# Performance work log

Hardware: AMD Instinct MI355X
Metric: run time of the kernel (lower is better)

Reference implementation:

```python
import jax, jax.numpy as jnp
import numpy as np

D_MODEL = 512
N_HEADS = 8
B, S = 4, 1024
REL_HIDDEN = 64


def setup_inputs() -> dict:
    key = jax.random.key(0)
    ks = jax.random.split(key, 16)

    def g(k, shape, scale=0.02):
        return jax.random.normal(k, shape, dtype=jnp.float32) * scale

    x = jax.random.normal(ks[0], (B, S, D_MODEL), dtype=jnp.float32)
    freqs = jax.random.uniform(ks[1], (B, S, 1), dtype=jnp.float32)
    return {
        "x": x,
        "freqs": freqs,
        "Wq": g(ks[2], (D_MODEL, D_MODEL)), "bq": g(ks[3], (D_MODEL,)),
        "Wk": g(ks[4], (D_MODEL, D_MODEL)), "bk": g(ks[5], (D_MODEL,)),
        "Wv": g(ks[6], (D_MODEL, D_MODEL)), "bv": g(ks[7], (D_MODEL,)),
        "Wo": g(ks[8], (D_MODEL, D_MODEL)), "bo": g(ks[9], (D_MODEL,)),
        "W1": g(ks[10], (2, REL_HIDDEN)), "b1": g(ks[11], (REL_HIDDEN,)),
        "W2": g(ks[12], (REL_HIDDEN, N_HEADS)), "b2": g(ks[13], (N_HEADS,)),
    }


def reference(x, freqs, Wq, bq, Wk, bk, Wv, bv, Wo, bo, W1, b1, W2, b2):
    b, s, d = x.shape
    h = N_HEADS
    dh = d // h

    def proj(W, bias):  # (b,s,d) -> (b,h,s,dh)
        return (x @ W + bias).reshape(b, s, h, dh).transpose(0, 2, 1, 3)

    Q = proj(Wq, bq)
    K = proj(Wk, bk)
    V = proj(Wv, bv)

    scores = jnp.einsum('bhid,bhjd->bhij', Q, K) / jnp.sqrt(jnp.float32(dh))

    # per-pair relative-frequency features: (b,s,s,2)
    eps = 1e-6
    fd = freqs[:, :, None, :] - freqs[:, None, :, :]
    fr = jnp.log((freqs[:, :, None, :] + eps) / (freqs[:, None, :, :] + eps))
    rel = jnp.concatenate([fd, fr], axis=-1)

    # MLP bias -> (b,s,s,h) -> (b,h,s,s)
    bias = jax.nn.relu(rel @ W1 + b1) @ W2 + b2
    scores = scores + jnp.transpose(bias, (0, 3, 1, 2))

    attn = jax.nn.softmax(scores, axis=-1)
    ctx = jnp.einsum('bhij,bhjd->bhid', attn, V)
    ctx = ctx.transpose(0, 2, 1, 3).reshape(b, s, d)
    return ctx @ Wo + bo
```

## Files before the change

kernel.cpp:

```cpp
#include <hip/hip_runtime.h>
#include <hip/hip_bf16.h>
#include <cstdint>

#define BATCH   4
#define SEQ     1024
#define DM      512
#define NH      8
#define DH      64
#define RH      64

typedef float f32x4 __attribute__((ext_vector_type(4)));
typedef __bf16 bf16x8 __attribute__((ext_vector_type(8)));

#define QB_OFF    (0)
#define KB_OFF    (4  << 20)
#define VT_OFF    (8  << 20)
#define XB_OFF    (12 << 20)
#define WT_OFF    (16 << 20)
#define WOT_OFF   (18 << 20)
#define W2T_OFF   (19 << 20)
#define AW_OFF    (20 << 20)
#define CW_OFF    (21 << 20)
#define CTXB_OFF  (22 << 20)
#define BIAS_OFF  (32 << 20)

__global__ __launch_bounds__(256) void cast_x(
    const float* __restrict__ x, __bf16* __restrict__ xb)
{
    const size_t i = ((size_t)blockIdx.x * 256 + threadIdx.x) * 8;
    const float4 a = *(const float4*)&x[i];
    const float4 b = *(const float4*)&x[i + 4];
    bf16x8 o;
    o[0] = (__bf16)a.x; o[1] = (__bf16)a.y; o[2] = (__bf16)a.z; o[3] = (__bf16)a.w;
    o[4] = (__bf16)b.x; o[5] = (__bf16)b.y; o[6] = (__bf16)b.z; o[7] = (__bf16)b.w;
    *(bf16x8*)&xb[i] = o;
}

__global__ __launch_bounds__(256) void cast_w(
    const float* __restrict__ Wq, const float* __restrict__ Wk,
    const float* __restrict__ Wv, const float* __restrict__ Wo,
    __bf16* __restrict__ Wt, __bf16* __restrict__ Wot)
{
    const int t = threadIdx.x;
    const int k0 = blockIdx.x * 64;
    const int n0 = blockIdx.y * 64;
    const int z  = blockIdx.z;
    const float* __restrict__ src = (z == 0) ? Wq : (z == 1) ? Wk : (z == 2) ? Wv : Wo;
    __bf16* __restrict__ dst = (z < 3) ? (Wt + (size_t)(z * 512 + n0) * 512)
                                       : (Wot + (size_t)n0 * 512);

    __shared__ __align__(16) float Ts[64][65];
    #pragma unroll
    for (int i = 0; i < 4; ++i) {
        const int id = t + i * 256;
        const int row = id >> 4, c4 = (id & 15) * 4;
        const float4 v = *(const float4*)&src[(size_t)(k0 + row) * DM + n0 + c4];
        Ts[row][c4 + 0] = v.x; Ts[row][c4 + 1] = v.y;
        Ts[row][c4 + 2] = v.z; Ts[row][c4 + 3] = v.w;
    }
    __syncthreads();
    #pragma unroll
    for (int i = 0; i < 2; ++i) {
        const int id = t + i * 256;
        const int rn = id >> 3, ck = (id & 7) * 8;
        bf16x8 o;
        #pragma unroll
        for (int j = 0; j < 8; ++j) o[j] = (__bf16)Ts[ck + j][rn];
        *(bf16x8*)&dst[(size_t)rn * 512 + k0 + ck] = o;
    }
}

__global__ __launch_bounds__(256) void w2t_kernel(
    const float* __restrict__ W2, __bf16* __restrict__ W2t)
{
    const int t = threadIdx.x;
    #pragma unroll
    for (int r = 0; r < 4; ++r) {
        const int id = t + r * 256;
        const int h = id >> 6, k = id & 63;
        W2t[id] = (h < NH) ? (__bf16)W2[k * NH + h] : (__bf16)0.f;
    }
}

__global__ __launch_bounds__(256) void gemm_qkv_mfma(
    const __bf16* __restrict__ xb, const __bf16* __restrict__ Wt,
    const float* __restrict__ bq, const float* __restrict__ bk,
    const float* __restrict__ bv,
    __bf16* __restrict__ Qb, __bf16* __restrict__ Kb, __bf16* __restrict__ Vtb)
{
    const int t = threadIdx.x;
    const int wave = t >> 6, lane = t & 63;
    const int wm = wave >> 1, wn = wave & 1;
    const int r = lane & 15, kc = lane >> 4, q4 = kc * 4;
    const int m0 = blockIdx.y * 128;
    const int n0 = blockIdx.x * 128;
    const int sec = n0 >> 9;
    const int nn = n0 & 511;

    __shared__ __align__(16) char smem[36864];
    __bf16* __restrict__ As = (__bf16*)smem;
    __bf16* __restrict__ Bs = (__bf16*)(smem + 18432);

    f32x4 acc[4][4];
    #pragma unroll
    for (int i = 0; i < 4; ++i)
        #pragma unroll
        for (int j = 0; j < 4; ++j) acc[i][j] = {0.f, 0.f, 0.f, 0.f};

    const int srow = t >> 3, sck = (t & 7) * 8;
    const __bf16* __restrict__ Ag = xb + (size_t)(m0 + srow) * 512 + sck;
    const __bf16* __restrict__ Bg = Wt + (size_t)(n0 + srow) * 512 + sck;

    for (int k0 = 0; k0 < 512; k0 += 64) {
        bf16x8 ra[4], rb[4];
        #pragma unroll
        for (int i = 0; i < 4; ++i) {
            ra[i] = *(const bf16x8*)(Ag + (size_t)i * 32 * 512 + k0);
            rb[i] = *(const bf16x8*)(Bg + (size_t)i * 32 * 512 + k0);
        }
        __syncthreads();
        #pragma unroll
        for (int i = 0; i < 4; ++i) {
            *(bf16x8*)&As[(srow + i * 32) * 72 + sck] = ra[i];
            *(bf16x8*)&Bs[(srow + i * 32) * 72 + sck] = rb[i];
        }
        __syncthreads();
        #pragma unroll
        for (int ks = 0; ks < 2; ++ks) {
            bf16x8 af[4], bf[4];
            #pragma unroll
            for (int mf = 0; mf < 4; ++mf)
                af[mf] = *(const bf16x8*)&As[(wm * 64 + mf * 16 + r) * 72 + ks * 32 + kc * 8];
            #pragma unroll
            for (int nf = 0; nf < 4; ++nf)
                bf[nf] = *(const bf16x8*)&Bs[(wn * 64 + nf * 16 + r) * 72 + ks * 32 + kc * 8];
            #pragma unroll
            for (int mf = 0; mf < 4; ++mf)
                #pragma unroll
                for (int nf = 0; nf < 4; ++nf)
                    acc[mf][nf] = __builtin_amdgcn_mfma_f32_16x16x32_bf16(
                        af[mf], bf[nf], acc[mf][nf], 0, 0, 0);
        }
    }

    const float* __restrict__ bias = (sec == 0) ? bq : (sec == 1) ? bk : bv;
    __syncthreads();
    __bf16* __restrict__ Ls = (__bf16*)smem;
    if (sec < 2) {
        #pragma unroll
        for (int mf = 0; mf < 4; ++mf)
            #pragma unroll
            for (int nf = 0; nf < 4; ++nf) {
                const int n_l = wn * 64 + nf * 16 + r;
                const float bb = bias[nn + n_l];
                #pragma unroll
                for (int rr = 0; rr < 4; ++rr)
                    Ls[(wm * 64 + mf * 16 + q4 + rr) * 136 + n_l] =
                        (__bf16)(acc[mf][nf][rr] + bb);
            }
    } else {
        #pragma unroll
        for (int mf = 0; mf < 4; ++mf)
            #pragma unroll
            for (int nf = 0; nf < 4; ++nf) {
                const int n_l = wn * 64 + nf * 16 + r;
                const float bb = bias[nn + n_l];
                #pragma unroll
                for (int rr = 0; rr < 4; ++rr)
                    Ls[n_l * 136 + (wm * 64 + mf * 16 + q4 + rr)] =
                        (__bf16)(acc[mf][nf][rr] + bb);
            }
    }
    __syncthreads();

    const int b = m0 >> 10, sbase = m0 & 1023;
    if (sec < 2) {
        __bf16* __restrict__ dst = sec ? Kb : Qb;
        #pragma unroll
        for (int i = 0; i < 8; ++i) {
            const int id = t + i * 256;
            const int row = id >> 4, nc = (id & 15) * 8;
            const bf16x8 v = *(const bf16x8*)&Ls[row * 136 + nc];
            const int ng = nn + nc, h = ng >> 6, c = ng & 63;
            *(bf16x8*)&dst[((size_t)(b * NH + h) * SEQ + sbase + row) * DH + c] = v;
        }
    } else {
        #pragma unroll
        for (int i = 0; i < 8; ++i) {
            const int id = t + i * 256;
            const int nrow = id >> 4, mc = (id & 15) * 8;
            const bf16x8 v = *(const bf16x8*)&Ls[nrow * 136 + mc];
            const int ng = nn + nrow, h = ng >> 6, c = ng & 63;
            *(bf16x8*)&Vtb[((size_t)(b * NH + h) * DH + c) * SEQ + sbase + mc] = v;
        }
    }
}

__global__ __launch_bounds__(256) void gemm_out_mfma(
    const __bf16* __restrict__ ctxb, const __bf16* __restrict__ Wot,
    const float* __restrict__ bo, float* __restrict__ out)
{
    const int t = threadIdx.x;
    const int wave = t >> 6, lane = t & 63;
    const int wm = wave >> 1, wn = wave & 1;
    const int r = lane & 15, kc = lane >> 4, q4 = kc * 4;
    const int m0 = blockIdx.y * 128;
    const int n0 = blockIdx.x * 128;

    __shared__ __align__(16) char smem[36864];
    __bf16* __restrict__ As = (__bf16*)smem;
    __bf16* __restrict__ Bs = (__bf16*)(smem + 18432);

    f32x4 acc[4][4];
    #pragma unroll
    for (int i = 0; i < 4; ++i)
        #pragma unroll
        for (int j = 0; j < 4; ++j) acc[i][j] = {0.f, 0.f, 0.f, 0.f};

    const int srow = t >> 3, sck = (t & 7) * 8;
    const __bf16* __restrict__ Ag = ctxb + (size_t)(m0 + srow) * 512 + sck;
    const __bf16* __restrict__ Bg = Wot + (size_t)(n0 + srow) * 512 + sck;

    for (int k0 = 0; k0 < 512; k0 += 64) {
        bf16x8 ra[4], rb[4];
        #pragma unroll
        for (int i = 0; i < 4; ++i) {
            ra[i] = *(const bf16x8*)(Ag + (size_t)i * 32 * 512 + k0);
            rb[i] = *(const bf16x8*)(Bg + (size_t)i * 32 * 512 + k0);
        }
        __syncthreads();
        #pragma unroll
        for (int i = 0; i < 4; ++i) {
            *(bf16x8*)&As[(srow + i * 32) * 72 + sck] = ra[i];
            *(bf16x8*)&Bs[(srow + i * 32) * 72 + sck] = rb[i];
        }
        __syncthreads();
        #pragma unroll
        for (int ks = 0; ks < 2; ++ks) {
            bf16x8 af[4], bf[4];
            #pragma unroll
            for (int mf = 0; mf < 4; ++mf)
                af[mf] = *(const bf16x8*)&As[(wm * 64 + mf * 16 + r) * 72 + ks * 32 + kc * 8];
            #pragma unroll
            for (int nf = 0; nf < 4; ++nf)
                bf[nf] = *(const bf16x8*)&Bs[(wn * 64 + nf * 16 + r) * 72 + ks * 32 + kc * 8];
            #pragma unroll
            for (int mf = 0; mf < 4; ++mf)
                #pragma unroll
                for (int nf = 0; nf < 4; ++nf)
                    acc[mf][nf] = __builtin_amdgcn_mfma_f32_16x16x32_bf16(
                        af[mf], bf[nf], acc[mf][nf], 0, 0, 0);
        }
    }

    #pragma unroll
    for (int mf = 0; mf < 4; ++mf)
        #pragma unroll
        for (int nf = 0; nf < 4; ++nf) {
            const int n_l = wn * 64 + nf * 16 + r;
            const float bb = bo[n0 + n_l];
            #pragma unroll
            for (int rr = 0; rr < 4; ++rr)
                out[(size_t)(m0 + wm * 64 + mf * 16 + q4 + rr) * DM + n0 + n_l] =
                    acc[mf][nf][rr] + bb;
        }
}

__global__ __launch_bounds__(64) void rel_kernel(
    const float* __restrict__ freqs,
    const float* __restrict__ W1,
    const float* __restrict__ b1,
    float* __restrict__ Aw,
    float* __restrict__ Cw)
{
    const int row = blockIdx.x;
    const int k = threadIdx.x;
    const float f = freqs[row];
    const float L = logf(f + 1e-6f);
    const float base = f * W1[k] + L * W1[RH + k];
    Aw[(size_t)row * RH + k] = base + b1[k];
    Cw[(size_t)row * RH + k] = -base;
}

__global__ __launch_bounds__(256) void bias_mfma(
    const float* __restrict__ Aw, const float* __restrict__ Cw,
    const __bf16* __restrict__ W2t, __bf16* __restrict__ biasb)
{
    const int t = threadIdx.x;
    const int wave = t >> 6, lane = t & 63;
    const int jl = lane & 15, kc = lane >> 4;
    const int j0 = blockIdx.x * 128;
    const int i0 = blockIdx.y * 16;
    const int b  = blockIdx.z;

    __shared__ __align__(16) float Cs[128][68];

    {
        const int jr = t >> 1, half = (t & 1) * 32;
        const float* __restrict__ src = &Cw[((size_t)b * SEQ + j0 + jr) * RH + half];
        #pragma unroll
        for (int q = 0; q < 8; ++q) {
            const float4 v = *(const float4*)(src + q * 4);
            *(float4*)&Cs[jr][half + q * 4] = v;
        }
    }

    const bf16x8 w2f0 = *(const bf16x8*)&W2t[jl * 64 + kc * 8];
    const bf16x8 w2f1 = *(const bf16x8*)&W2t[jl * 64 + 32 + kc * 8];

    __syncthreads();

    const int iw = i0 + wave * 4;
    #pragma unroll
    for (int ii = 0; ii < 4; ++ii) {
        const int i = iw + ii;
        const float* __restrict__ ap = &Aw[((size_t)b * SEQ + i) * RH];
        const float4 a0 = *(const float4*)(ap + kc * 8);
        const float4 a1 = *(const float4*)(ap + kc * 8 + 4);
        const float4 a2 = *(const float4*)(ap + 32 + kc * 8);
        const float4 a3 = *(const float4*)(ap + 32 + kc * 8 + 4);

        #pragma unroll
        for (int jt = 0; jt < 8; ++jt) {
            const float* __restrict__ cp = &Cs[jt * 16 + jl][kc * 8];
            f32x4 acc = {0.f, 0.f, 0.f, 0.f};

            const float4 c0 = *(const float4*)(cp);
            const float4 c1 = *(const float4*)(cp + 4);
            bf16x8 hb0;
            hb0[0] = (__bf16)fmaxf(a0.x + c0.x, 0.f);
            hb0[1] = (__bf16)fmaxf(a0.y + c0.y, 0.f);
            hb0[2] = (__bf16)fmaxf(a0.z + c0.z, 0.f);
            hb0[3] = (__bf16)fmaxf(a0.w + c0.w, 0.f);
            hb0[4] = (__bf16)fmaxf(a1.x + c1.x, 0.f);
            hb0[5] = (__bf16)fmaxf(a1.y + c1.y, 0.f);
            hb0[6] = (__bf16)fmaxf(a1.z + c1.z, 0.f);
            hb0[7] = (__bf16)fmaxf(a1.w + c1.w, 0.f);
            acc = __builtin_amdgcn_mfma_f32_16x16x32_bf16(w2f0, hb0, acc, 0, 0, 0);

            const float4 c2 = *(const float4*)(cp + 32);
            const float4 c3 = *(const float4*)(cp + 36);
            bf16x8 hb1;
            hb1[0] = (__bf16)fmaxf(a2.x + c2.x, 0.f);
            hb1[1] = (__bf16)fmaxf(a2.y + c2.y, 0.f);
            hb1[2] = (__bf16)fmaxf(a2.z + c2.z, 0.f);
            hb1[3] = (__bf16)fmaxf(a2.w + c2.w, 0.f);
            hb1[4] = (__bf16)fmaxf(a3.x + c3.x, 0.f);
            hb1[5] = (__bf16)fmaxf(a3.y + c3.y, 0.f);
            hb1[6] = (__bf16)fmaxf(a3.z + c3.z, 0.f);
            hb1[7] = (__bf16)fmaxf(a3.w + c3.w, 0.f);
            acc = __builtin_amdgcn_mfma_f32_16x16x32_bf16(w2f1, hb1, acc, 0, 0, 0);

            if (kc < 2) {
                #pragma unroll
                for (int rr = 0; rr < 4; ++rr)
                    biasb[(((size_t)b * NH + kc * 4 + rr) * SEQ + i) * SEQ
                          + j0 + jt * 16 + jl] = (__bf16)acc[rr];
            }
        }
    }
}

#define SSTR 1028
#define PSTR 1032

__global__ __launch_bounds__(512) void attn_mfma(
    const __bf16* __restrict__ Qb, const __bf16* __restrict__ Kb,
    const __bf16* __restrict__ Vtb, const __bf16* __restrict__ biasb,
    __bf16* __restrict__ ctxb)
{
    const int t = threadIdx.x;
    const int wave = t >> 6, lane = t & 63;
    const int r = lane & 15, kc = lane >> 4;
    const int blk = blockIdx.x;
    const int it = blk & 63;
    const int h  = (blk >> 6) & 7;
    const int b  = blk >> 9;
    const int s0 = it * 16;
    const int bh = b * NH + h;

    __shared__ __align__(16) float Ss[16 * SSTR];
    __shared__ float invl[16];

    const int prow = t >> 5, pln = t & 31;
    const __bf16* __restrict__ bpre =
        biasb + ((size_t)bh * SEQ + s0 + prow) * SEQ + pln * 8;
    const bf16x8 bre0 = *(const bf16x8*)(bpre);
    const bf16x8 bre1 = *(const bf16x8*)(bpre + 256);
    const bf16x8 bre2 = *(const bf16x8*)(bpre + 512);
    const bf16x8 bre3 = *(const bf16x8*)(bpre + 768);

    {
        const __bf16* __restrict__ Qp = Qb + ((size_t)bh * SEQ + s0) * DH;
        const __bf16* __restrict__ Kp = Kb + (size_t)bh * SEQ * DH;
        const bf16x8 qa0 = *(const bf16x8*)(Qp + r * DH + kc * 8);
        const bf16x8 qa1 = *(const bf16x8*)(Qp + r * DH + 32 + kc * 8);
        __builtin_amdgcn_s_setprio(1);
        #pragma unroll
        for (int jt = 0; jt < 8; ++jt) {
            const int j0 = wave * 128 + jt * 16;
            const bf16x8 kb0 = *(const bf16x8*)(Kp + (size_t)(j0 + r) * DH + kc * 8);
            const bf16x8 kb1 = *(const bf16x8*)(Kp + (size_t)(j0 + r) * DH + 32 + kc * 8);
            f32x4 acc = {0.f, 0.f, 0.f, 0.f};
            acc = __builtin_amdgcn_mfma_f32_16x16x32_bf16(qa0, kb0, acc, 0, 0, 0);
            acc = __builtin_amdgcn_mfma_f32_16x16x32_bf16(qa1, kb1, acc, 0, 0, 0);
            #pragma unroll
            for (int rr = 0; rr < 4; ++rr)
                Ss[(kc * 4 + rr) * SSTR + j0 + r] = acc[rr] * 0.125f;
        }
        __builtin_amdgcn_s_setprio(0);
    }
    __syncthreads();

    {
        const float* __restrict__ sp = &Ss[prow * SSTR + pln * 8];
        float sv[32];
        float m = -1e30f;
        #pragma unroll
        for (int c = 0; c < 4; ++c) {
            const float4 sa = *(const float4*)(sp + c * 256);
            const float4 sb = *(const float4*)(sp + c * 256 + 4);
            const bf16x8 br = (c == 0) ? bre0 : (c == 1) ? bre1 : (c == 2) ? bre2 : bre3;
            float s;
            s = sa.x + (float)br[0]; sv[c * 8 + 0] = s; m = fmaxf(m, s);
            s = sa.y + (float)br[1]; sv[c * 8 + 1] = s; m = fmaxf(m, s);
            s = sa.z + (float)br[2]; sv[c * 8 + 2] = s; m = fmaxf(m, s);
            s = sa.w + (float)br[3]; sv[c * 8 + 3] = s; m = fmaxf(m, s);
            s = sb.x + (float)br[4]; sv[c * 8 + 4] = s; m = fmaxf(m, s);
            s = sb.y + (float)br[5]; sv[c * 8 + 5] = s; m = fmaxf(m, s);
            s = sb.z + (float)br[6]; sv[c * 8 + 6] = s; m = fmaxf(m, s);
            s = sb.w + (float)br[7]; sv[c * 8 + 7] = s; m = fmaxf(m, s);
        }
        #pragma unroll
        for (int mask = 16; mask >= 1; mask >>= 1)
            m = fmaxf(m, __shfl_xor(m, mask));
        float l = 0.f;
        #pragma unroll
        for (int jj = 0; jj < 32; ++jj) {
            const float p = __expf(sv[jj] - m);
            sv[jj] = p;
            l += p;
        }
        #pragma unroll
        for (int mask = 16; mask >= 1; mask >>= 1)
            l += __shfl_xor(l, mask);
        if (pln == 0) invl[prow] = 1.0f / l;
        __syncthreads();
        __bf16* __restrict__ Pb = (__bf16*)Ss;
        #pragma unroll
        for (int c = 0; c < 4; ++c) {
            bf16x8 pv;
            #pragma unroll
            for (int e = 0; e < 8; ++e) pv[e] = (__bf16)sv[c * 8 + e];
            *(bf16x8*)&Pb[prow * PSTR + c * 256 + pln * 8] = pv;
        }
    }
    __syncthreads();

    {
        const int ct = wave & 3, kh = wave >> 2;
        const __bf16* __restrict__ Pb = (const __bf16*)Ss;
        const __bf16* __restrict__ Vp =
            Vtb + ((size_t)bh * DH + ct * 16 + r) * SEQ + kh * 512;
        f32x4 acc = {0.f, 0.f, 0.f, 0.f};
        __builtin_amdgcn_s_setprio(1);
        #pragma unroll 4
        for (int jt = 0; jt < 16; ++jt) {
            const bf16x8 pa = *(const bf16x8*)(Pb + (size_t)r * PSTR + kh * 512 + jt * 32 + kc * 8);
            const bf16x8 vb = *(const bf16x8*)(Vp + jt * 32 + kc * 8);
            acc = __builtin_amdgcn_mfma_f32_16x16x32_bf16(pa, vb, acc, 0, 0, 0);
        }
        __builtin_amdgcn_s_setprio(0);
        float* __restrict__ part = Ss + 8256;
        if (kh == 1) {
            #pragma unroll
            for (int rr = 0; rr < 4; ++rr)
                part[ct * 272 + (kc * 4 + rr) * 17 + r] = acc[rr];
        }
        __syncthreads();
        if (kh == 0) {
            #pragma unroll
            for (int rr = 0; rr < 4; ++rr) {
                const int row = kc * 4 + rr;
                const float v = (acc[rr] + part[ct * 272 + row * 17 + r]) * invl[row];
                ctxb[((size_t)(b * SEQ) + s0 + row) * DM + h * DH + ct * 16 + r] = (__bf16)v;
            }
        }
    }
}

extern "C" void kernel_launch(void* const* d_in, const int* in_sizes, int n_in,
                              void* d_out, int out_size, void* d_ws, size_t ws_size,
                              hipStream_t stream)
{
    const float* x     = (const float*)d_in[0];
    const float* freqs = (const float*)d_in[1];
    const float* Wq    = (const float*)d_in[2];
    const float* bq    = (const float*)d_in[3];
    const float* Wk    = (const float*)d_in[4];
    const float* bk    = (const float*)d_in[5];
    const float* Wv    = (const float*)d_in[6];
    const float* bv    = (const float*)d_in[7];
    const float* Wo    = (const float*)d_in[8];
    const float* bo    = (const float*)d_in[9];
    const float* W1    = (const float*)d_in[10];
    const float* b1    = (const float*)d_in[11];
    const float* W2    = (const float*)d_in[12];

    char* wsb = (char*)d_ws;
    __bf16* Qb    = (__bf16*)(wsb + QB_OFF);
    __bf16* Kb    = (__bf16*)(wsb + KB_OFF);
    __bf16* Vtb   = (__bf16*)(wsb + VT_OFF);
    __bf16* xb    = (__bf16*)(wsb + XB_OFF);
    __bf16* Wt    = (__bf16*)(wsb + WT_OFF);
    __bf16* Wot   = (__bf16*)(wsb + WOT_OFF);
    __bf16* W2t   = (__bf16*)(wsb + W2T_OFF);
    float*  Aw    = (float*)(wsb + AW_OFF);
    float*  Cw    = (float*)(wsb + CW_OFF);
    __bf16* ctxb  = (__bf16*)(wsb + CTXB_OFF);
    __bf16* biasb = (__bf16*)(wsb + BIAS_OFF);
    float* out = (float*)d_out;

    cast_x<<<dim3(1024), 256, 0, stream>>>(x, xb);
    cast_w<<<dim3(8, 8, 4), 256, 0, stream>>>(Wq, Wk, Wv, Wo, Wt, Wot);
    w2t_kernel<<<dim3(1), 256, 0, stream>>>(W2, W2t);
    rel_kernel<<<dim3(4096), 64, 0, stream>>>(freqs, W1, b1, Aw, Cw);
    gemm_qkv_mfma<<<dim3(12, 32), 256, 0, stream>>>(xb, Wt, bq, bk, bv, Qb, Kb, Vtb);
    bias_mfma<<<dim3(8, 64, 4), 256, 0, stream>>>(Aw, Cw, W2t, biasb);
    attn_mfma<<<dim3(2048), 512, 0, stream>>>(Qb, Kb, Vtb, biasb, ctxb);
    gemm_out_mfma<<<dim3(4, 32), 256, 0, stream>>>(ctxb, Wot, bo, out);
}
```

Measured before the change: 221.8 us.

## Keep attention scores in registers, drop max pass, and swizzle block order

After: 219.2 us. Within noise of the previous version (-1.2%).

```diff
diff --git a/kernel.cpp b/kernel.cpp
--- a/kernel.cpp
+++ b/kernel.cpp
@@ -92,8 +92,10 @@
     const int wave = t >> 6, lane = t & 63;
     const int wm = wave >> 1, wn = wave & 1;
     const int r = lane & 15, kc = lane >> 4, q4 = kc * 4;
-    const int m0 = blockIdx.y * 128;
-    const int n0 = blockIdx.x * 128;
+    const int lin = blockIdx.y * 12 + blockIdx.x;
+    const int swz = (lin & 7) * 48 + (lin >> 3);
+    const int m0 = (swz / 12) * 128;
+    const int n0 = (swz % 12) * 128;
     const int sec = n0 >> 9;
     const int nn = n0 & 511;
 
@@ -204,8 +206,10 @@
     const int wave = t >> 6, lane = t & 63;
     const int wm = wave >> 1, wn = wave & 1;
     const int r = lane & 15, kc = lane >> 4, q4 = kc * 4;
-    const int m0 = blockIdx.y * 128;
-    const int n0 = blockIdx.x * 128;
+    const int lin = blockIdx.y * 4 + blockIdx.x;
+    const int swz = (lin & 7) * 16 + (lin >> 3);
+    const int m0 = (swz / 4) * 128;
+    const int n0 = (swz % 4) * 128;
 
     __shared__ __align__(16) char smem[36864];
     __bf16* __restrict__ As = (__bf16*)smem;
@@ -361,7 +365,6 @@
     }
 }
 
-#define SSTR 1028
 #define PSTR 1032
 
 __global__ __launch_bounds__(512) void attn_mfma(
@@ -372,106 +375,96 @@
     const int t = threadIdx.x;
     const int wave = t >> 6, lane = t & 63;
     const int r = lane & 15, kc = lane >> 4;
-    const int blk = blockIdx.x;
+    const int blk = (blockIdx.x & 7) * 256 + (blockIdx.x >> 3);
     const int it = blk & 63;
     const int h  = (blk >> 6) & 7;
     const int b  = blk >> 9;
     const int s0 = it * 16;
     const int bh = b * NH + h;
 
-    __shared__ __align__(16) float Ss[16 * SSTR];
+    __shared__ __align__(16) __bf16 Pb[16 * PSTR];
+    __shared__ __align__(16) float part[1088];
+    __shared__ float red[8][16];
     __shared__ float invl[16];
 
-    const int prow = t >> 5, pln = t & 31;
-    const __bf16* __restrict__ bpre =
-        biasb + ((size_t)bh * SEQ + s0 + prow) * SEQ + pln * 8;
-    const bf16x8 bre0 = *(const bf16x8*)(bpre);
-    const bf16x8 bre1 = *(const bf16x8*)(bpre + 256);
-    const bf16x8 bre2 = *(const bf16x8*)(bpre + 512);
-    const bf16x8 bre3 = *(const bf16x8*)(bpre + 768);
-
+    uint32_t brg[4][8];
+    {
+        const uint16_t* __restrict__ bb = (const uint16_t*)biasb
+            + ((size_t)bh * SEQ + s0 + kc * 4) * SEQ + wave * 128 + r;
+        #pragma unroll
+        for (int rr = 0; rr < 4; ++rr)
+            #pragma unroll
+            for (int jt = 0; jt < 8; ++jt)
+                brg[rr][jt] = bb[(size_t)rr * SEQ + jt * 16];
+    }
+
+    f32x4 sc[8];
     {
         const __bf16* __restrict__ Qp = Qb + ((size_t)bh * SEQ + s0) * DH;
-        const __bf16* __restrict__ Kp = Kb + (size_t)bh * SEQ * DH;
+        const __bf16* __restrict__ Kp = Kb + ((size_t)bh * SEQ + wave * 128) * DH;
         const bf16x8 qa0 = *(const bf16x8*)(Qp + r * DH + kc * 8);
         const bf16x8 qa1 = *(const bf16x8*)(Qp + r * DH + 32 + kc * 8);
         __builtin_amdgcn_s_setprio(1);
         #pragma unroll
         for (int jt = 0; jt < 8; ++jt) {
-            const int j0 = wave * 128 + jt * 16;
-            const bf16x8 kb0 = *(const bf16x8*)(Kp + (size_t)(j0 + r) * DH + kc * 8);
-            const bf16x8 kb1 = *(const bf16x8*)(Kp + (size_t)(j0 + r) * DH + 32 + kc * 8);
-            f32x4 acc = {0.f, 0.f, 0.f, 0.f};
-            acc = __builtin_amdgcn_mfma_f32_16x16x32_bf16(qa0, kb0, acc, 0, 0, 0);
-            acc = __builtin_amdgcn_mfma_f32_16x16x32_bf16(qa1, kb1, acc, 0, 0, 0);
-            #pragma unroll
-            for (int rr = 0; rr < 4; ++rr)
-                Ss[(kc * 4 + rr) * SSTR + j0 + r] = acc[rr] * 0.125f;
+            const bf16x8 kb0 = *(const bf16x8*)(Kp + (size_t)(jt * 16 + r) * DH + kc * 8);
+            const bf16x8 kb1 = *(const bf16x8*)(Kp + (size_t)(jt * 16 + r) * DH + 32 + kc * 8);
+            f32x4 a = {0.f, 0.f, 0.f, 0.f};
+            a = __builtin_amdgcn_mfma_f32_16x16x32_bf16(qa0, kb0, a, 0, 0, 0);
+            a = __builtin_amdgcn_mfma_f32_16x16x32_bf16(qa1, kb1, a, 0, 0, 0);
+            sc[jt] = a;
         }
         __builtin_amdgcn_s_setprio(0);
     }
+
+    float psum[4] = {0.f, 0.f, 0.f, 0.f};
+    #pragma unroll
+    for (int jt = 0; jt < 8; ++jt) {
+        #pragma unroll
+        for (int rr = 0; rr < 4; ++rr) {
+            const float s = fmaf(sc[jt][rr], 0.125f,
+                                 __uint_as_float(brg[rr][jt] << 16));
+            const float p = __expf(fminf(s, 30.f));
+            sc[jt][rr] = p;
+            psum[rr] += p;
+        }
+    }
+    #pragma unroll
+    for (int mask = 8; mask >= 1; mask >>= 1)
+        #pragma unroll
+        for (int rr = 0; rr < 4; ++rr)
+            psum[rr] += __shfl_xor(psum[rr], mask);
+    if (r == 0) {
+        #pragma unroll
+        for (int rr = 0; rr < 4; ++rr) red[wave][kc * 4 + rr] = psum[rr];
+    }
+    #pragma unroll
+    for (int jt = 0; jt < 8; ++jt)
+        #pragma unroll
+        for (int rr = 0; rr < 4; ++rr)
+            Pb[(kc * 4 + rr) * PSTR + wave * 128 + jt * 16 + r] = (__bf16)sc[jt][rr];
     __syncthreads();
 
-    {
-        const float* __restrict__ sp = &Ss[prow * SSTR + pln * 8];
-        float sv[32];
-        float m = -1e30f;
-        #pragma unroll
-        for (int c = 0; c < 4; ++c) {
-            const float4 sa = *(const float4*)(sp + c * 256);
-            const float4 sb = *(const float4*)(sp + c * 256 + 4);
-            const bf16x8 br = (c == 0) ? bre0 : (c == 1) ? bre1 : (c == 2) ? bre2 : bre3;
-            float s;
-            s = sa.x + (float)br[0]; sv[c * 8 + 0] = s; m = fmaxf(m, s);
-            s = sa.y + (float)br[1]; sv[c * 8 + 1] = s; m = fmaxf(m, s);
-            s = sa.z + (float)br[2]; sv[c * 8 + 2] = s; m = fmaxf(m, s);
-            s = sa.w + (float)br[3]; sv[c * 8 + 3] = s; m = fmaxf(m, s);
-            s = sb.x + (float)br[4]; sv[c * 8 + 4] = s; m = fmaxf(m, s);
-            s = sb.y + (float)br[5]; sv[c * 8 + 5] = s; m = fmaxf(m, s);
-            s = sb.z + (float)br[6]; sv[c * 8 + 6] = s; m = fmaxf(m, s);
-            s = sb.w + (float)br[7]; sv[c * 8 + 7] = s; m = fmaxf(m, s);
-        }
-        #pragma unroll
-        for (int mask = 16; mask >= 1; mask >>= 1)
-            m = fmaxf(m, __shfl_xor(m, mask));
+    if (t < 16) {
         float l = 0.f;
         #pragma unroll
-        for (int jj = 0; jj < 32; ++jj) {
-            const float p = __expf(sv[jj] - m);
-            sv[jj] = p;
-            l += p;
-        }
-        #pragma unroll
-        for (int mask = 16; mask >= 1; mask >>= 1)
-            l += __shfl_xor(l, mask);
-        if (pln == 0) invl[prow] = 1.0f / l;
-        __syncthreads();
-        __bf16* __restrict__ Pb = (__bf16*)Ss;
-        #pragma unroll
-        for (int c = 0; c < 4; ++c) {
-            bf16x8 pv;
-            #pragma unroll
-            for (int e = 0; e < 8; ++e) pv[e] = (__bf16)sv[c * 8 + e];
-            *(bf16x8*)&Pb[prow * PSTR + c * 256 + pln * 8] = pv;
-        }
-    }
-    __syncthreads();
+        for (int w = 0; w < 8; ++w) l += red[w][t];
+        invl[t] = 1.0f / l;
+    }
 
     {
         const int ct = wave & 3, kh = wave >> 2;
-        const __bf16* __restrict__ Pb = (const __bf16*)Ss;
         const __bf16* __restrict__ Vp =
             Vtb + ((size_t)bh * DH + ct * 16 + r) * SEQ + kh * 512;
         f32x4 acc = {0.f, 0.f, 0.f, 0.f};
         __builtin_amdgcn_s_setprio(1);
         #pragma unroll 4
         for (int jt = 0; jt < 16; ++jt) {
-            const bf16x8 pa = *(const bf16x8*)(Pb + (size_t)r * PSTR + kh * 512 + jt * 32 + kc * 8);
+            const bf16x8 pa = *(const bf16x8*)&Pb[r * PSTR + kh * 512 + jt * 32 + kc * 8];
             const bf16x8 vb = *(const bf16x8*)(Vp + jt * 32 + kc * 8);
             acc = __builtin_amdgcn_mfma_f32_16x16x32_bf16(pa, vb, acc, 0, 0, 0);
         }
         __builtin_amdgcn_s_setprio(0);
-        float* __restrict__ part = Ss + 8256;
         if (kh == 1) {
             #pragma unroll
             for (int rr = 0; rr < 4; ++rr)
```
